# Kernel tuning notes

Hardware: AMD Instinct MI355X
Metric: run time of the kernel (lower is better)

Reference implementation:

```python
import jax, jax.numpy as jnp
import numpy as np

N = 100000      # nodes
E = 1600000     # directed edges (before self loops)
F_IN = 3        # node_feature_dim
H = 32          # hidden_dim
BN_EPS = 1e-5


def _linear_params(k, fan_in, fan_out):
    lim = 1.0 / np.sqrt(fan_in)
    kw, kb = jax.random.split(k)
    W = jax.random.uniform(kw, (fan_in, fan_out), jnp.float32, -lim, lim)
    b = jax.random.uniform(kb, (fan_out,), jnp.float32, -lim, lim)
    return W, b


def setup_inputs() -> dict:
    key = jax.random.key(0)
    ks = jax.random.split(key, 12)
    x = jax.random.normal(ks[0], (N, F_IN), jnp.float32)
    edge_index = jax.random.randint(ks[1], (2, E), 0, N, dtype=jnp.int64)
    node_type = jax.random.randint(ks[2], (N,), 0, 3, dtype=jnp.int64)
    W1, b1 = _linear_params(ks[3], F_IN, H)
    W2, b2 = _linear_params(ks[4], H, H)
    W3, b3 = _linear_params(ks[5], H, H)
    g1 = jnp.ones((H,), jnp.float32); be1 = jnp.zeros((H,), jnp.float32)
    g2 = jnp.ones((H,), jnp.float32); be2 = jnp.zeros((H,), jnp.float32)
    Wc1, bc1 = _linear_params(ks[6], H, H // 2)
    Wc2, bc2 = _linear_params(ks[7], H // 2, 1)
    Wd1, bd1 = _linear_params(ks[8], H, H // 2)
    Wd2, bd2 = _linear_params(ks[9], H // 2, 1)
    return dict(x=x, edge_index=edge_index, node_type=node_type,
                W1=W1, b1=b1, W2=W2, b2=b2, W3=W3, b3=b3,
                g1=g1, be1=be1, g2=g2, be2=be2,
                Wc1=Wc1, bc1=bc1, Wc2=Wc2, bc2=bc2,
                Wd1=Wd1, bd1=bd1, Wd2=Wd2, bd2=bd2)


def reference(x, edge_index, node_type, W1, b1, W2, b2, W3, b3,
              g1, be1, g2, be2, Wc1, bc1, Wc2, bc2, Wd1, bd1, Wd2, bd2):
    n = x.shape[0]
    # GCNConv (PyG default): add self loops, symmetric deg^-1/2 normalization
    loop = jnp.arange(n, dtype=edge_index.dtype)
    src = jnp.concatenate([edge_index[0], loop])  # [E+N]
    dst = jnp.concatenate([edge_index[1], loop])
    deg = jax.ops.segment_sum(jnp.ones_like(dst, dtype=x.dtype), dst, num_segments=n)
    dinv = jnp.where(deg > 0, jax.lax.rsqrt(jnp.maximum(deg, 1.0)), 0.0)
    norm = dinv[src] * dinv[dst]  # [E+N]

    def conv(h, W, b):
        msg = (h @ W)[src] * norm[:, None]                  # gather + scale
        return jax.ops.segment_sum(msg, dst, num_segments=n) + b  # scatter-add

    def bn(h, g, be):  # BatchNorm1d with batch statistics (training math)
        mu = h.mean(axis=0)
        var = ((h - mu) ** 2).mean(axis=0)
        return (h - mu) * jax.lax.rsqrt(var + BN_EPS) * g + be

    h = bn(jax.nn.relu(conv(x, W1, b1)), g1, be1)   # dropout = identity (eval)
    h = bn(jax.nn.relu(conv(h, W2, b2)), g2, be2)
    h = jax.nn.relu(conv(h, W3, b3))

    cand_mask = node_type == 0
    cand_emb = h[cand_mask]                                 # [C, H]
    cand_scores = (jax.nn.relu(cand_emb @ Wc1 + bc1) @ Wc2 + bc2)[:, 0]

    w = jax.nn.softmax(h.sum(axis=1))[:, None]              # [N,1] importance
    g_emb = (h * w).sum(axis=0, keepdims=True)              # [1, H]
    dn = (jax.nn.relu(g_emb @ Wd1 + bd1) @ Wd2 + bd2).reshape(())

    logits = jnp.concatenate([cand_scores, dn[None]], axis=0)
    cand_idx = jnp.nonzero(cand_mask)[0]
    return logits, cand_idx
```

## Files before the change

kernel.cpp:

```cpp
#include <hip/hip_runtime.h>

typedef unsigned int uint;
typedef unsigned char uchar;

#define NB_MAX 256
#define NPB_MAX 2048

static __device__ __forceinline__ uint f2fp8(float v) {
    v = fminf(fmaxf(v, -448.f), 448.f);
    uint u = __float_as_uint(v);
    uint s = (u >> 24) & 0x80u;
    uint mag = u & 0x7FFFFFFFu;
    uint r = mag + 0x7FFFFu + ((mag >> 20) & 1u);
    if (r < 0x3C800000u) return s;
    uint e8 = (r - 0x3C000000u) >> 20;
    return s | min(e8, 0x7Eu);
}
static __device__ __forceinline__ float fp82f(uint b) {
    uint mag = b & 0x7Fu;
    uint bits = ((b & 0x80u) << 24) | ((mag << 20) + 0x3C000000u);
    return mag ? __uint_as_float(bits) : 0.f;
}
static __device__ __forceinline__ void dec8(uint2 v, float* o) {
    o[0]=fp82f(v.x&0xFF); o[1]=fp82f((v.x>>8)&0xFF); o[2]=fp82f((v.x>>16)&0xFF); o[3]=fp82f(v.x>>24);
    o[4]=fp82f(v.y&0xFF); o[5]=fp82f((v.y>>8)&0xFF); o[6]=fp82f((v.y>>16)&0xFF); o[7]=fp82f(v.y>>24);
}
static __device__ __forceinline__ uint2 enc8(const float* o) {
    uint2 r;
    r.x = f2fp8(o[0]) | (f2fp8(o[1])<<8) | (f2fp8(o[2])<<16) | (f2fp8(o[3])<<24);
    r.y = f2fp8(o[4]) | (f2fp8(o[5])<<8) | (f2fp8(o[6])<<16) | (f2fp8(o[7])<<24);
    return r;
}
static __device__ __forceinline__ void dec32(const uchar* row, float* o) {
    const uint4* r4 = (const uint4*)row;
    uint4 A = r4[0], B = r4[1];
    dec8(make_uint2(A.x,A.y), o); dec8(make_uint2(A.z,A.w), o+8);
    dec8(make_uint2(B.x,B.y), o+16); dec8(make_uint2(B.z,B.w), o+24);
}
static __device__ __forceinline__ void enc32(const float* o, uchar* row) {
    uint2 a = enc8(o), b = enc8(o+8), c = enc8(o+16), d = enc8(o+24);
    uint4* r4 = (uint4*)row;
    r4[0] = make_uint4(a.x,a.y,b.x,b.y);
    r4[1] = make_uint4(c.x,c.y,d.x,d.y);
}

static __device__ __forceinline__ unsigned wave_incl_scan(unsigned v) {
    int lane = threadIdx.x & 63;
    #pragma unroll
    for (int d = 1; d < 64; d <<= 1) {
        unsigned t = (unsigned)__shfl_up((int)v, d, 64);
        if (lane >= d) v += t;
    }
    return v;
}

static __device__ void block_excl_scan(const uint* in, uint* out, int n, uint* wscr) {
    int tid = threadIdx.x;
    int lane = tid & 63, wid = tid >> 6;
    int base = tid * 8;
    uint v[8], pre[8], s = 0;
    #pragma unroll
    for (int k = 0; k < 8; k++) v[k] = (base + k < n) ? in[base + k] : 0u;
    #pragma unroll
    for (int k = 0; k < 8; k++) { pre[k] = s; s += v[k]; }
    uint is = wave_incl_scan(s);
    __syncthreads();
    if (lane == 63) wscr[wid] = is;
    __syncthreads();
    uint woff = 0;
    for (int wI = 0; wI < wid; wI++) woff += wscr[wI];
    uint excl = is - s + woff;
    #pragma unroll
    for (int k = 0; k < 8; k++) if (base + k < n) out[base + k] = excl + pre[k];
    __syncthreads();
}

__global__ __launch_bounds__(256) void bucket_hist_kernel(const int* src, const int* dst,
                                                          const int* nt, uint* bcnt, uint* bcand,
                                                          int E, int N, int NB, int shift) {
    __shared__ uint bh[NB_MAX], ch[NB_MAX];
    int tid = threadIdx.x;
    bh[tid] = 0; ch[tid] = 0;
    __syncthreads();
    int gs = gridDim.x * 256;
    for (int i = blockIdx.x * 256 + tid; i < E; i += gs) {
        int d = dst[i], s = src[i];
        if ((uint)d < (uint)N && (uint)s < (uint)N) atomicAdd(&bh[d >> shift], 1u);
    }
    for (int i = blockIdx.x * 256 + tid; i < N; i += gs) {
        if (nt[i] == 0) atomicAdd(&ch[i >> shift], 1u);
    }
    __syncthreads();
    if (bh[tid]) atomicAdd(&bcnt[tid], bh[tid]);
    if (ch[tid]) atomicAdd(&bcand[tid], ch[tid]);
}

__global__ __launch_bounds__(256) void partition_kernel(const int* src, const int* dst,
                                                        const uint* bcnt, uint* alloc0,
                                                        uint* staging, int E, int N, int shift) {
    __shared__ uint bbase_s[NB_MAX];
    __shared__ uint lh[NB_MAX], gb[NB_MAX];
    __shared__ uint ws4[4];
    int tid = threadIdx.x;
    int lane = tid & 63, wid = tid >> 6;
    uint a = bcnt[tid];
    uint ia = wave_incl_scan(a);
    if (lane == 63) ws4[wid] = ia;
    __syncthreads();
    uint off = 0;
    for (int wI = 0; wI < wid; wI++) off += ws4[wI];
    bbase_s[tid] = ia - a + off;
    lh[tid] = 0;
    __syncthreads();
    int base = blockIdx.x * 2048;
    uint mask = (1u << shift) - 1u;
    int breg[8];
    uint rreg[8], pk8[8];
    #pragma unroll
    for (int k = 0; k < 8; k++) {
        int e = base + k * 256 + tid;
        breg[k] = -1;
        if (e < E) {
            int s = src[e], d = dst[e];
            if ((uint)d < (uint)N && (uint)s < (uint)N) {
                int b = d >> shift;
                pk8[k] = (((uint)d & mask) << 17) | (uint)s;
                breg[k] = b;
                rreg[k] = atomicAdd(&lh[b], 1u);
            }
        }
    }
    __syncthreads();
    gb[tid] = lh[tid] ? (bbase_s[tid] + atomicAdd(&alloc0[tid], lh[tid])) : 0u;
    __syncthreads();
    #pragma unroll
    for (int k = 0; k < 8; k++) {
        if (breg[k] >= 0)
            staging[gb[breg[k]] + rreg[k]] = pk8[k];
    }
}

__global__ __launch_bounds__(256) void local_csr_kernel(const uint* staging, const uint* bcnt,
                                                        const uint* bcand, const int* nt,
                                                        const float* x, const float* W1,
                                                        int* csr_src, uint* csr_off, uint* cand_pos,
                                                        float* dinv, uchar* zb,
                                                        int N, int shift, int NB) {
    __shared__ uint deg[NPB_MAX];
    __shared__ uint ofs[NPB_MAX];
    __shared__ uint ws4[4];
    __shared__ uint sb[4];
    __shared__ float Ws[96];
    int b = blockIdx.x, tid = threadIdx.x;
    int lane = tid & 63, wid = tid >> 6;
    if (tid < 96) Ws[tid] = W1[tid];
    uint a = bcnt[tid];
    uint ia = wave_incl_scan(a);
    if (lane == 63) ws4[wid] = ia;
    __syncthreads();
    uint off = 0;
    for (int wI = 0; wI < wid; wI++) off += ws4[wI];
    if (tid == b) { sb[0] = ia - a + off; sb[1] = ia + off; }
    __syncthreads();
    uint c = bcand[tid];
    uint ic = wave_incl_scan(c);
    if (lane == 63) ws4[wid] = ic;
    __syncthreads();
    uint offc = 0;
    for (int wI = 0; wI < wid; wI++) offc += ws4[wI];
    if (tid == b) sb[2] = ic - c + offc;
    __syncthreads();
    uint ebase = sb[0], eend = sb[1], cb = sb[2];
    int nbase = b << shift;
    int ncount = min(1 << shift, N - nbase);
    for (int i = tid; i < ncount; i += 256) deg[i] = 0;
    __syncthreads();
    for (uint p = ebase + tid; p < eend; p += 256)
        atomicAdd(&deg[staging[p] >> 17], 1u);
    __syncthreads();
    block_excl_scan(deg, ofs, ncount, ws4);
    for (int i = tid; i < ncount; i += 256)
        csr_off[nbase + i] = ebase + ofs[i];
    if (b == NB - 1 && tid == 0) csr_off[N] = eend;
    for (int i = tid; i < ncount; i += 256) {
        int g = nbase + i;
        float di = rsqrtf((float)(deg[i] + 1u));
        dinv[g] = di;
        float x0 = x[3 * g], x1 = x[3 * g + 1], x2 = x[3 * g + 2];
        float o[32];
        #pragma unroll
        for (int j = 0; j < 32; j++)
            o[j] = (x0 * Ws[j] + x1 * Ws[32 + j] + x2 * Ws[64 + j]) * di;
        enc32(o, zb + (size_t)g * 32);
    }
    __syncthreads();
    for (int i = tid; i < ncount; i += 256) deg[i] = 0;
    __syncthreads();
    for (uint p = ebase + tid; p < eend; p += 256) {
        uint pkv = staging[p];
        uint dl = pkv >> 17;
        uint pos = ebase + ofs[dl] + atomicAdd(&deg[dl], 1u);
        csr_src[pos] = (int)(pkv & 0x1FFFFu);
    }
    __syncthreads();
    for (int i = tid; i < ncount; i += 256) deg[i] = (nt[nbase + i] == 0) ? 1u : 0u;
    __syncthreads();
    block_excl_scan(deg, ofs, ncount, ws4);
    for (int i = tid; i < ncount; i += 256) cand_pos[nbase + i] = cb + ofs[i];
}

__global__ __launch_bounds__(256) void gemmf_kernel(const uchar* hb, const float* stats_sum,
                                                    const float* stats_sq, const float* g,
                                                    const float* be, const float* W,
                                                    const float* dinv, uchar* zb, int n,
                                                    float inv_n) {
    __shared__ float Ws[1024];
    __shared__ float cs[32];
    __shared__ float a_s[32], d_s[32];
    int tid = threadIdx.x;
    if (tid < 32) {
        float mu = stats_sum[tid] * inv_n;
        float var = fmaxf(stats_sq[tid] * inv_n - mu * mu, 0.f);
        float a = g[tid] * rsqrtf(var + 1e-5f);
        a_s[tid] = a;
        d_s[tid] = be[tid] - mu * a;
    }
    __syncthreads();
    #pragma unroll
    for (int t = tid; t < 1024; t += 256) Ws[t] = a_s[t >> 5] * W[t];
    if (tid < 32) {
        float c = 0.f;
        for (int k = 0; k < 32; k++) c += d_s[k] * W[k * 32 + tid];
        cs[tid] = c;
    }
    __syncthreads();
    int i = blockIdx.x * 256 + tid;
    if (i >= n) return;
    float hk[32], acc[32];
    dec32(hb + (size_t)i * 32, hk);
    #pragma unroll
    for (int j = 0; j < 32; j++) acc[j] = cs[j];
    #pragma unroll
    for (int k = 0; k < 32; k++) {
        float h0 = hk[k];
        #pragma unroll
        for (int j = 0; j < 32; j++) acc[j] += h0 * Ws[k * 32 + j];
    }
    float di = dinv[i];
    #pragma unroll
    for (int j = 0; j < 32; j++) acc[j] *= di;
    enc32(acc, zb + (size_t)i * 32);
}

__global__ __launch_bounds__(256) void agg_kernel(const uchar* zb, const int* csr_src,
                                                  const uint* csr_off, const float* dinv,
                                                  const float* bias, uchar* hb, int n,
                                                  int mode, float* stats_sum, float* stats_sq,
                                                  float* rowsum, uint* maxkey) {
    const int tid = threadIdx.x;
    const int wave = tid >> 6;
    const int lane = tid & 63;
    const int c4 = lane & 3;
    const int slot = lane >> 2;
    float bs[8], bq[8];
    #pragma unroll
    for (int j = 0; j < 8; j++) { bs[j] = 0.f; bq[j] = 0.f; }
    float lmax = -3.0e38f;
    int node = (blockIdx.x * 4 + wave) * 16 + slot;
    if (node < n) {
        uint s = csr_off[node], e = csr_off[node + 1];
        float acc[8];
        dec8(*(const uint2*)(zb + (size_t)node * 32 + c4 * 8), acc);
        for (uint p = s; p < e; p += 8) {
            uint idx[8];
            float wg[8];
            #pragma unroll
            for (int j = 0; j < 8; j++) {
                uint q = p + (uint)j;
                uint qc = min(q, e - 1u);
                idx[j] = (uint)csr_src[qc];
                wg[j] = (q < e) ? 1.f : 0.f;
            }
            #pragma unroll
            for (int j = 0; j < 8; j++) {
                float t[8];
                dec8(*(const uint2*)(zb + (size_t)idx[j] * 32 + c4 * 8), t);
                #pragma unroll
                for (int cI = 0; cI < 8; cI++) acc[cI] = fmaf(wg[j], t[cI], acc[cI]);
            }
        }
        float di = dinv[node];
        float hv[8];
        #pragma unroll
        for (int j = 0; j < 8; j++) hv[j] = fmaxf(di * acc[j] + bias[c4 * 8 + j], 0.f);
        *(uint2*)(hb + (size_t)node * 32 + c4 * 8) = enc8(hv);
        if (mode == 0) {
            #pragma unroll
            for (int j = 0; j < 8; j++) { bs[j] = hv[j]; bq[j] = hv[j] * hv[j]; }
        } else {
            float rs = ((hv[0] + hv[1]) + (hv[2] + hv[3])) + ((hv[4] + hv[5]) + (hv[6] + hv[7]));
            rs += __shfl_xor(rs, 1, 64);
            rs += __shfl_xor(rs, 2, 64);
            if (c4 == 0) { rowsum[node] = rs; lmax = rs; }
        }
    }
    if (mode == 0) {
        #pragma unroll
        for (int m = 4; m < 64; m <<= 1) {
            #pragma unroll
            for (int j = 0; j < 8; j++) {
                bs[j] += __shfl_xor(bs[j], m, 64);
                bq[j] += __shfl_xor(bq[j], m, 64);
            }
        }
        __shared__ float ssum[4][32], ssq[4][32];
        if (slot == 0) {
            #pragma unroll
            for (int j = 0; j < 8; j++) { ssum[wave][c4 * 8 + j] = bs[j]; ssq[wave][c4 * 8 + j] = bq[j]; }
        }
        __syncthreads();
        if (tid < 32) {
            atomicAdd(&stats_sum[tid], ssum[0][tid] + ssum[1][tid] + ssum[2][tid] + ssum[3][tid]);
            atomicAdd(&stats_sq[tid],  ssq[0][tid] + ssq[1][tid] + ssq[2][tid] + ssq[3][tid]);
        }
    } else {
        #pragma unroll
        for (int m = 1; m < 64; m <<= 1) lmax = fmaxf(lmax, __shfl_xor(lmax, m, 64));
        __shared__ float lm[4];
        if (lane == 0) lm[wave] = lmax;
        __syncthreads();
        if (tid == 0) {
            float m = fmaxf(fmaxf(lm[0], lm[1]), fmaxf(lm[2], lm[3]));
            uint u = __float_as_uint(m);
            uint key = (u & 0x80000000u) ? ~u : (u | 0x80000000u);
            atomicMax(maxkey, key);
        }
    }
}

__global__ __launch_bounds__(256) void head_kernel(const uchar* hb, const int* nt,
                                                   const uint* pos, const float* Wc1,
                                                   const float* bc1, const float* Wc2,
                                                   const float* bc2, const float* rowsum,
                                                   const uint* maxkey, float* gvec, float* Zp,
                                                   uint* ticket, const float* Wd1,
                                                   const float* bd1, const float* Wd2,
                                                   const float* bd2, float* out, int n, int C) {
    __shared__ float W1s[512], b1s[16], W2s[16];
    __shared__ float ls[256];
    __shared__ float ge[32], tt[16];
    __shared__ int lastflag;
    int tid = threadIdx.x;
    for (int t = tid; t < 512; t += 256) W1s[t] = Wc1[t];
    if (tid < 16) { b1s[tid] = bc1[tid]; W2s[tid] = Wc2[tid]; }
    __syncthreads();
    int i = blockIdx.x * 256 + tid;
    if (i < n && nt[i] == 0) {
        float hv[32];
        dec32(hb + (size_t)i * 32, hv);
        float s = bc2[0];
        #pragma unroll
        for (int j = 0; j < 16; j++) {
            float u = b1s[j];
            #pragma unroll
            for (int k = 0; k < 32; k++) u += hv[k] * W1s[k * 16 + j];
            s += fmaxf(u, 0.f) * W2s[j];
        }
        s = fminf(fmaxf(s, -1000.f), 1000.f);
        uint p = pos[i];
        if (p < (uint)C) {
            out[p] = s;
            out[C + 1 + p] = (float)i;
        }
    }
    uint key = *maxkey;
    float M = 0.f;
    if (key != 0u) M = (key & 0x80000000u) ? __uint_as_float(key ^ 0x80000000u) : __uint_as_float(~key);
    int lane = tid & 31, grp = tid >> 5;
    int stride = gridDim.x * 8;
    float accZ = 0.f, accg = 0.f;
    for (int node = blockIdx.x * 8 + grp; node < n; node += stride) {
        float ew = __expf(rowsum[node] - M);
        accg += fp82f(hb[(size_t)node * 32 + lane]) * ew;
        if (lane == 0) accZ += ew;
    }
    ls[tid] = accg;
    __syncthreads();
    if (tid < 32) {
        float a = 0.f;
        #pragma unroll
        for (int g = 0; g < 8; g++) a += ls[tid + 32 * g];
        atomicAdd(&gvec[tid], a);
    }
    __syncthreads();
    ls[tid] = (lane == 0) ? accZ : 0.f;
    __syncthreads();
    if (tid == 0) {
        float a = 0.f;
        for (int t = 0; t < 256; t += 32) a += ls[t];
        atomicAdd(Zp, a);
        __threadfence();
        uint old = atomicAdd(ticket, 1u);
        lastflag = (old == gridDim.x - 1) ? 1 : 0;
    }
    __syncthreads();
    if (lastflag) {
        __threadfence();
        if (tid < 32) ge[tid] = atomicAdd(&gvec[tid], 0.f);
        if (tid == 0) ls[0] = atomicAdd(Zp, 0.f);
        __syncthreads();
        float Zv = fmaxf(ls[0], 1e-30f);
        if (tid < 32) ge[tid] /= Zv;
        __syncthreads();
        if (tid < 16) {
            float s = bd1[tid];
            for (int k = 0; k < 32; k++) s += ge[k] * Wd1[k * 16 + tid];
            tt[tid] = fmaxf(s, 0.f);
        }
        __syncthreads();
        if (tid == 0) {
            float s = bd2[0];
            for (int j = 0; j < 16; j++) s += tt[j] * Wd2[j];
            out[C] = fminf(fmaxf(s, -1000.f), 1000.f);
        }
    }
}

extern "C" void kernel_launch(void* const* d_in, const int* in_sizes, int n_in,
                              void* d_out, int out_size, void* d_ws, size_t ws_size,
                              hipStream_t stream) {
    const float* x   = (const float*)d_in[0];
    const int*   ei  = (const int*)d_in[1];
    const int*   nt  = (const int*)d_in[2];
    const float* W1  = (const float*)d_in[3];  const float* b1  = (const float*)d_in[4];
    const float* W2  = (const float*)d_in[5];  const float* b2  = (const float*)d_in[6];
    const float* W3  = (const float*)d_in[7];  const float* b3  = (const float*)d_in[8];
    const float* g1  = (const float*)d_in[9];  const float* be1 = (const float*)d_in[10];
    const float* g2  = (const float*)d_in[11]; const float* be2 = (const float*)d_in[12];
    const float* Wc1 = (const float*)d_in[13]; const float* bc1 = (const float*)d_in[14];
    const float* Wc2 = (const float*)d_in[15]; const float* bc2 = (const float*)d_in[16];
    const float* Wd1 = (const float*)d_in[17]; const float* bd1 = (const float*)d_in[18];
    const float* Wd2 = (const float*)d_in[19]; const float* bd2 = (const float*)d_in[20];

    const int N = in_sizes[0] / 3;
    const int E = in_sizes[1] / 2;
    const int C = (out_size - 1) / 2;
    const int* e_src = ei;
    const int* e_dst = ei + E;
    float* out = (float*)d_out;

    int shift = 9;
    while (((N + (1 << shift) - 1) >> shift) > NB_MAX) shift++;
    const int NB = (N + (1 << shift) - 1) >> shift;

    char* w = (char*)d_ws;
    auto alloc = [&](size_t bytes) { void* p = (void*)w; w += (bytes + 255) & ~(size_t)255; return p; };
    float*    stats  = (float*)alloc(256 * 4);
    uint*     bcnt   = (uint*)alloc(NB_MAX * 4);
    uint*     bcand  = (uint*)alloc(NB_MAX * 4);
    uint*     alloc0 = (uint*)alloc(NB_MAX * 4);
    size_t zero_bytes = (size_t)((char*)w - (char*)stats);
    float*    dinv   = (float*)alloc((size_t)N * 4);
    uint*     csr_off= (uint*)alloc((size_t)(N + 1) * 4);
    uint*     cand_pos=(uint*)alloc((size_t)N * 4);
    float*    rowsum = (float*)alloc((size_t)N * 4);
    int*      csr_src= (int*)alloc((size_t)E * 4);
    uint*     staging= (uint*)alloc((size_t)E * 4);
    uchar*    zb     = (uchar*)alloc((size_t)N * 32);
    uchar*    hb     = (uchar*)alloc((size_t)N * 32);

    float* sum1 = stats;       float* sq1 = stats + 32;
    float* sum2 = stats + 64;  float* sq2 = stats + 96;
    float* gvec = stats + 128; float* Zp  = stats + 160;
    uint* maxkey = (uint*)(stats + 161);
    uint* ticket = (uint*)(stats + 162);

    hipMemsetAsync(stats, 0, zero_bytes, stream);

    const int gN   = (N + 255) / 256;
    const int gPar = (E + 2047) / 2048;
    const int gAgg = (N + 63) / 64;
    const float inv_n = 1.0f / (float)N;

    hipLaunchKernelGGL(bucket_hist_kernel, dim3(784), dim3(256), 0, stream, e_src, e_dst, nt, bcnt, bcand, E, N, NB, shift);
    hipLaunchKernelGGL(partition_kernel, dim3(gPar), dim3(256), 0, stream, e_src, e_dst, bcnt, alloc0, staging, E, N, shift);
    hipLaunchKernelGGL(local_csr_kernel, dim3(NB), dim3(256), 0, stream, staging, bcnt, bcand, nt,
                       x, W1, csr_src, csr_off, cand_pos, dinv, zb, N, shift, NB);

    hipLaunchKernelGGL(agg_kernel, dim3(gAgg), dim3(256), 0, stream, zb, csr_src, csr_off,
                       dinv, b1, hb, N, 0, sum1, sq1, rowsum, maxkey);

    hipLaunchKernelGGL(gemmf_kernel, dim3(gN), dim3(256), 0, stream, hb, sum1, sq1, g1, be1, W2, dinv, zb, N, inv_n);
    hipLaunchKernelGGL(agg_kernel, dim3(gAgg), dim3(256), 0, stream, zb, csr_src, csr_off,
                       dinv, b2, hb, N, 0, sum2, sq2, rowsum, maxkey);

    hipLaunchKernelGGL(gemmf_kernel, dim3(gN), dim3(256), 0, stream, hb, sum2, sq2, g2, be2, W3, dinv, zb, N, inv_n);
    hipLaunchKernelGGL(agg_kernel, dim3(gAgg), dim3(256), 0, stream, zb, csr_src, csr_off,
                       dinv, b3, hb, N, 1, sum1, sq1, rowsum, maxkey);

    hipLaunchKernelGGL(head_kernel, dim3(gN), dim3(256), 0, stream, hb, nt, cand_pos,
                       Wc1, bc1, Wc2, bc2, rowsum, maxkey, gvec, Zp, ticket,
                       Wd1, bd1, Wd2, bd2, out, N, C);
}
```

Before: 372.3 us.

## Use hardware FP8 conversions and dynamic per-block node scheduling in aggregation

Swaps the software FP8 encode/decode for the AMD packed fp8 conversion builtins when the compiler provides them, which cuts ALU work on every gathered neighbour row. The aggregation kernel now has each 4-lane group pull nodes from a 128-node chunk through a shared atomic counter, so work is balanced across groups despite uneven degrees. Statistics now accumulate over several nodes per lane. Grid size is halved to match the 128-node chunks. Risks: the hardware FP8 format's rounding and saturation may differ from the software e4m3 path, and the extra atomics and block barriers add overhead.

```diff
diff --git a/kernel.cpp b/kernel.cpp
--- a/kernel.cpp
+++ b/kernel.cpp
@@ -6,7 +6,15 @@
 #define NB_MAX 256
 #define NPB_MAX 2048
 
-static __device__ __forceinline__ uint f2fp8(float v) {
+#if defined(__has_builtin)
+#if __has_builtin(__builtin_amdgcn_cvt_pk_f32_fp8) && __has_builtin(__builtin_amdgcn_cvt_pk_fp8_f32)
+#define HW_FP8 1
+#endif
+#endif
+
+typedef __attribute__((ext_vector_type(2))) float v2f;
+
+static __device__ __forceinline__ uint f2fp8_sw(float v) {
     v = fminf(fmaxf(v, -448.f), 448.f);
     uint u = __float_as_uint(v);
     uint s = (u >> 24) & 0x80u;
@@ -22,14 +30,31 @@
     return mag ? __uint_as_float(bits) : 0.f;
 }
 static __device__ __forceinline__ void dec8(uint2 v, float* o) {
+#ifdef HW_FP8
+    v2f a = __builtin_amdgcn_cvt_pk_f32_fp8((int)v.x, false);
+    v2f b = __builtin_amdgcn_cvt_pk_f32_fp8((int)v.x, true);
+    v2f c = __builtin_amdgcn_cvt_pk_f32_fp8((int)v.y, false);
+    v2f d = __builtin_amdgcn_cvt_pk_f32_fp8((int)v.y, true);
+    o[0]=a.x; o[1]=a.y; o[2]=b.x; o[3]=b.y;
+    o[4]=c.x; o[5]=c.y; o[6]=d.x; o[7]=d.y;
+#else
     o[0]=fp82f(v.x&0xFF); o[1]=fp82f((v.x>>8)&0xFF); o[2]=fp82f((v.x>>16)&0xFF); o[3]=fp82f(v.x>>24);
     o[4]=fp82f(v.y&0xFF); o[5]=fp82f((v.y>>8)&0xFF); o[6]=fp82f((v.y>>16)&0xFF); o[7]=fp82f(v.y>>24);
+#endif
 }
 static __device__ __forceinline__ uint2 enc8(const float* o) {
+#ifdef HW_FP8
+    int rx = __builtin_amdgcn_cvt_pk_fp8_f32(o[0], o[1], 0, false);
+    rx = __builtin_amdgcn_cvt_pk_fp8_f32(o[2], o[3], rx, true);
+    int ry = __builtin_amdgcn_cvt_pk_fp8_f32(o[4], o[5], 0, false);
+    ry = __builtin_amdgcn_cvt_pk_fp8_f32(o[6], o[7], ry, true);
+    return make_uint2((uint)rx, (uint)ry);
+#else
     uint2 r;
-    r.x = f2fp8(o[0]) | (f2fp8(o[1])<<8) | (f2fp8(o[2])<<16) | (f2fp8(o[3])<<24);
-    r.y = f2fp8(o[4]) | (f2fp8(o[5])<<8) | (f2fp8(o[6])<<16) | (f2fp8(o[7])<<24);
+    r.x = f2fp8_sw(o[0]) | (f2fp8_sw(o[1])<<8) | (f2fp8_sw(o[2])<<16) | (f2fp8_sw(o[3])<<24);
+    r.y = f2fp8_sw(o[4]) | (f2fp8_sw(o[5])<<8) | (f2fp8_sw(o[6])<<16) | (f2fp8_sw(o[7])<<24);
     return r;
+#endif
 }
 static __device__ __forceinline__ void dec32(const uchar* row, float* o) {
     const uint4* r4 = (const uint4*)row;
@@ -262,47 +287,62 @@
     const int lane = tid & 63;
     const int c4 = lane & 3;
     const int slot = lane >> 2;
+    const int qlead = lane & ~3;
+    __shared__ uint s_lt;
+    float bv[8];
+    #pragma unroll
+    for (int j = 0; j < 8; j++) bv[j] = bias[c4 * 8 + j];
     float bs[8], bq[8];
     #pragma unroll
     for (int j = 0; j < 8; j++) { bs[j] = 0.f; bq[j] = 0.f; }
     float lmax = -3.0e38f;
-    int node = (blockIdx.x * 4 + wave) * 16 + slot;
-    if (node < n) {
-        uint s = csr_off[node], e = csr_off[node + 1];
-        float acc[8];
-        dec8(*(const uint2*)(zb + (size_t)node * 32 + c4 * 8), acc);
-        for (uint p = s; p < e; p += 8) {
-            uint idx[8];
-            float wg[8];
+    for (uint cbase = (uint)blockIdx.x * 128u; cbase < (uint)n; cbase += gridDim.x * 128u) {
+        uint avail = min((uint)n - cbase, 128u);
+        if (tid == 0) s_lt = 0u;
+        __syncthreads();
+        while (true) {
+            uint li = 0;
+            if (c4 == 0) li = atomicAdd(&s_lt, 1u);
+            li = (uint)__shfl((int)li, qlead, 64);
+            if (li >= avail) break;
+            uint node = cbase + li;
+            uint s = csr_off[node], e = csr_off[node + 1];
+            float acc[8];
+            dec8(*(const uint2*)(zb + (size_t)node * 32 + c4 * 8), acc);
+            for (uint p = s; p < e; p += 8) {
+                uint idx[8];
+                float wg[8];
+                #pragma unroll
+                for (int j = 0; j < 8; j++) {
+                    uint q = p + (uint)j;
+                    uint qc = min(q, e - 1u);
+                    idx[j] = (uint)csr_src[qc];
+                    wg[j] = (q < e) ? 1.f : 0.f;
+                }
+                #pragma unroll
+                for (int j = 0; j < 8; j++) {
+                    float t[8];
+                    dec8(*(const uint2*)(zb + (size_t)idx[j] * 32 + c4 * 8), t);
+                    #pragma unroll
+                    for (int cI = 0; cI < 8; cI++) acc[cI] = fmaf(wg[j], t[cI], acc[cI]);
+                }
+            }
+            float di = dinv[node];
+            float hv[8];
             #pragma unroll
-            for (int j = 0; j < 8; j++) {
-                uint q = p + (uint)j;
-                uint qc = min(q, e - 1u);
-                idx[j] = (uint)csr_src[qc];
-                wg[j] = (q < e) ? 1.f : 0.f;
+            for (int j = 0; j < 8; j++) hv[j] = fmaxf(di * acc[j] + bv[j], 0.f);
+            *(uint2*)(hb + (size_t)node * 32 + c4 * 8) = enc8(hv);
+            if (mode == 0) {
+                #pragma unroll
+                for (int j = 0; j < 8; j++) { bs[j] += hv[j]; bq[j] += hv[j] * hv[j]; }
+            } else {
+                float rs = ((hv[0] + hv[1]) + (hv[2] + hv[3])) + ((hv[4] + hv[5]) + (hv[6] + hv[7]));
+                rs += __shfl_xor(rs, 1, 64);
+                rs += __shfl_xor(rs, 2, 64);
+                if (c4 == 0) { rowsum[node] = rs; lmax = fmaxf(lmax, rs); }
             }
-            #pragma unroll
-            for (int j = 0; j < 8; j++) {
-                float t[8];
-                dec8(*(const uint2*)(zb + (size_t)idx[j] * 32 + c4 * 8), t);
-                #pragma unroll
-                for (int cI = 0; cI < 8; cI++) acc[cI] = fmaf(wg[j], t[cI], acc[cI]);
-            }
-        }
-        float di = dinv[node];
-        float hv[8];
-        #pragma unroll
-        for (int j = 0; j < 8; j++) hv[j] = fmaxf(di * acc[j] + bias[c4 * 8 + j], 0.f);
-        *(uint2*)(hb + (size_t)node * 32 + c4 * 8) = enc8(hv);
-        if (mode == 0) {
-            #pragma unroll
-            for (int j = 0; j < 8; j++) { bs[j] = hv[j]; bq[j] = hv[j] * hv[j]; }
-        } else {
-            float rs = ((hv[0] + hv[1]) + (hv[2] + hv[3])) + ((hv[4] + hv[5]) + (hv[6] + hv[7]));
-            rs += __shfl_xor(rs, 1, 64);
-            rs += __shfl_xor(rs, 2, 64);
-            if (c4 == 0) { rowsum[node] = rs; lmax = rs; }
-        }
+        }
+        __syncthreads();
     }
     if (mode == 0) {
         #pragma unroll
@@ -479,7 +519,7 @@
 
     const int gN   = (N + 255) / 256;
     const int gPar = (E + 2047) / 2048;
-    const int gAgg = (N + 63) / 64;
+    const int gAgg = (N + 127) / 128;
     const float inv_n = 1.0f / (float)N;
 
     hipLaunchKernelGGL(bucket_hist_kernel, dim3(784), dim3(256), 0, stream, e_src, e_dst, nt, bcnt, bcand, E, N, NB, shift);
```

After: 332.3 us. -10.7%, faster.
